# Performance work log

Hardware: AMD Instinct MI355X
Metric: run time of the kernel (lower is better)

Reference implementation:

```python
import jax, jax.numpy as jnp
import numpy as np

D = 1024  # d_model

def setup_inputs() -> dict:
    key = jax.random.key(0)
    ks = jax.random.split(key, 12)
    s = 1.0 / np.sqrt(D)  # torch Linear default init scale
    inp = {
        "q": jax.random.normal(ks[0], (4, 4096, D), dtype=jnp.float32),
        "k": jax.random.normal(ks[1], (4, 4096, D), dtype=jnp.float32),
        "v": jax.random.normal(ks[2], (4, 4096, D), dtype=jnp.float32),
        "Wq": jax.random.uniform(ks[3], (D, D), jnp.float32, -s, s),
        "bq": jax.random.uniform(ks[4], (D,), jnp.float32, -s, s),
        "Wk": jax.random.uniform(ks[5], (D, D), jnp.float32, -s, s),
        "bk": jax.random.uniform(ks[6], (D,), jnp.float32, -s, s),
        "Wv": jax.random.uniform(ks[7], (D, D), jnp.float32, -s, s),
        "bv": jax.random.uniform(ks[8], (D,), jnp.float32, -s, s),
        "Wo": jax.random.uniform(ks[9], (D, D), jnp.float32, -s, s),
        "bo": jax.random.uniform(ks[10], (D,), jnp.float32, -s, s),
    }
    return inp

def reference(q, k, v, Wq, bq, Wk, bk, Wv, bv, Wo, bo):
    # phi feature map: exp(-x^2 / 2)
    phi = lambda x: jnp.exp(-0.5 * x * x)
    Q = phi(q @ Wq.T + bq)            # [B, N, D]
    K = phi(k @ Wk.T + bk)            # [B, N, D]
    V = v @ Wv.T + bv                 # [B, N, D]
    # linear attention: aggregate K^T V once, then contract with Q
    KV = jnp.einsum('bnd,bnl->bdl', K, V)                 # [B, D, D]
    Z = 1.0 / (jnp.einsum('bnd,bd->bn', Q, K.sum(axis=1)) + 1e-6)  # [B, N]
    out = jnp.einsum('bnd,bdl->bnl', Q, KV) * Z[..., None]         # [B, N, D]
    return out @ Wo.T + bo
```

## Files before the change

kernel.cpp:

```cpp
#include <hip/hip_runtime.h>

typedef unsigned short u16;
typedef unsigned int u32;
typedef unsigned long long u64;

typedef __attribute__((ext_vector_type(8))) short short8;
typedef __attribute__((ext_vector_type(4))) float floatx4;

__device__ __forceinline__ float b2f(u16 h) {
  u32 u = ((u32)h) << 16;
  return __builtin_bit_cast(float, u);
}
__device__ __forceinline__ u16 f2b(float f) {
  u32 u = __builtin_bit_cast(u32, f);
  u32 r = 0x7FFFu + ((u >> 16) & 1u);
  return (u16)((u + r) >> 16);
}

__device__ __forceinline__ void gl_lds16(const void* g, void* l) {
  __builtin_amdgcn_global_load_lds(
      (__attribute__((address_space(1))) void*)(u64)g,
      (__attribute__((address_space(3))) void*)(u32)(u64)l, 16, 0, 0);
}

enum { EPI_PHI_BIAS = 0, EPI_BIAS = 1, EPI_NONE = 2,
       EPI_ZBIAS_F32 = 3 };

template<int EPI, bool TRANS_OUT>
__global__ __launch_bounds__(512, 2)
void gemm_bt256(const u16* __restrict__ Ap, const u16* __restrict__ Bp0,
                const float* __restrict__ bias, const float* __restrict__ Zall,
                void* __restrict__ Cp,
                int M, int N, int K, int ldA, int ldB, int ldC,
                long sAb, long sBb, long sCb, long sZb, int abmask, int kshift)
{
  constexpr int TSTRIDE = 65536;
  constexpr int BOFF    = 32768;
  __shared__ char smem[2 * TSTRIDE];

  const int tid  = threadIdx.x;
  const int lane = tid & 63;
  const int wave = tid >> 6;
  const int wm = wave >> 2, wn = wave & 3;
  const int fl = lane & 15;
  const int q  = lane >> 4;
  const int r4 = q * 4;
  const int bm0 = blockIdx.x * 256, bn0 = blockIdx.y * 256;
  const int bz = blockIdx.z;
  const int abz = bz & abmask;
  const int kbase = (bz >> kshift) * K;

  const u16* Ah = Ap  + (size_t)abz * sAb + kbase;
  const u16* Bh = Bp0 + (size_t)abz * sBb + kbase;

  const u16* gA[4]; const u16* gB[4]; int sL[4];
  #pragma unroll
  for (int n = 0; n < 4; ++n) {
    int j = n * 512 + tid;
    int R = j >> 3, c = (j & 7) ^ (R & 7);
    gA[n] = Ah + (size_t)(bm0 + R) * ldA + c * 8;
    gB[n] = Bh + (size_t)(bn0 + R) * ldB + c * 8;
    sL[n] = (n * 512 + wave * 64) * 16;
  }

  int aoff[8], boff[4];
  #pragma unroll
  for (int i = 0; i < 8; ++i) {
    int ra = wm * 128 + i * 16 + fl;
    aoff[i] = ra * 128 + ((q ^ (ra & 7)) * 16);
  }
  #pragma unroll
  for (int i = 0; i < 4; ++i) {
    int rb = wn * 64 + i * 16 + fl;
    boff[i] = rb * 128 + ((q ^ (rb & 7)) * 16);
  }

  floatx4 zero = {0.f, 0.f, 0.f, 0.f};
  floatx4 acc[8][4];
  #pragma unroll
  for (int i = 0; i < 8; ++i)
    #pragma unroll
    for (int j = 0; j < 4; ++j) acc[i][j] = zero;

  auto stage = [&](int t, char* base) {
    int k0 = t * 64;
    #pragma unroll
    for (int n = 0; n < 4; ++n) gl_lds16(gA[n] + k0, base + sL[n]);
    #pragma unroll
    for (int n = 0; n < 4; ++n) gl_lds16(gB[n] + k0, base + BOFF + sL[n]);
  };

  const int NT = K >> 6;
  stage(0, smem);
  asm volatile("s_waitcnt vmcnt(0)\ns_barrier" ::: "memory");
  int cur = 0;
  for (int t = 0; t < NT; ++t) {
    const bool pf = t + 1 < NT;
    const char* bufc = smem + cur;
    char* stb = smem + (cur ^ TSTRIDE);
    const int k1 = (t + 1) * 64;
    short8 aL[8], aH[8], b01[4], b23[4];

    #pragma unroll
    for (int i = 0; i < 4; ++i) {
      aL[2 * i]     = *(const short8*)(bufc + aoff[i]);
      aL[2 * i + 1] = *(const short8*)(bufc + (aoff[i] ^ 64));
    }
    #pragma unroll
    for (int i = 0; i < 2; ++i) {
      b01[2 * i]     = *(const short8*)(bufc + BOFF + boff[i]);
      b01[2 * i + 1] = *(const short8*)(bufc + BOFF + (boff[i] ^ 64));
    }
    if (pf) {
      #pragma unroll
      for (int n = 0; n < 4; ++n) gl_lds16(gA[n] + k1, stb + sL[n]);
    }
    __builtin_amdgcn_s_barrier();
    asm volatile("s_waitcnt lgkmcnt(0)" ::: "memory");
    __builtin_amdgcn_sched_barrier(0);
    __builtin_amdgcn_s_setprio(1);
    #pragma unroll
    for (int kk = 0; kk < 2; ++kk)
      #pragma unroll
      for (int mi = 0; mi < 4; ++mi)
        #pragma unroll
        for (int ni = 0; ni < 2; ++ni)
          acc[mi][ni] = __builtin_amdgcn_mfma_f32_16x16x32_bf16(
              aL[2 * mi + kk], b01[2 * ni + kk], acc[mi][ni], 0, 0, 0);
    __builtin_amdgcn_s_setprio(0);
    __builtin_amdgcn_s_barrier();

    #pragma unroll
    for (int i = 0; i < 2; ++i) {
      b23[2 * i]     = *(const short8*)(bufc + BOFF + boff[i + 2]);
      b23[2 * i + 1] = *(const short8*)(bufc + BOFF + (boff[i + 2] ^ 64));
    }
    if (pf) {
      #pragma unroll
      for (int n = 0; n < 4; ++n) gl_lds16(gB[n] + k1, stb + BOFF + sL[n]);
    }
    __builtin_amdgcn_s_barrier();
    asm volatile("s_waitcnt lgkmcnt(0)" ::: "memory");
    __builtin_amdgcn_sched_barrier(0);
    __builtin_amdgcn_s_setprio(1);
    #pragma unroll
    for (int kk = 0; kk < 2; ++kk)
      #pragma unroll
      for (int mi = 0; mi < 4; ++mi)
        #pragma unroll
        for (int ni = 0; ni < 2; ++ni)
          acc[mi][ni + 2] = __builtin_amdgcn_mfma_f32_16x16x32_bf16(
              aL[2 * mi + kk], b23[2 * ni + kk], acc[mi][ni + 2], 0, 0, 0);
    __builtin_amdgcn_s_setprio(0);
    __builtin_amdgcn_s_barrier();

    #pragma unroll
    for (int i = 0; i < 4; ++i) {
      aH[2 * i]     = *(const short8*)(bufc + aoff[i + 4]);
      aH[2 * i + 1] = *(const short8*)(bufc + (aoff[i + 4] ^ 64));
    }
    __builtin_amdgcn_s_barrier();
    asm volatile("s_waitcnt lgkmcnt(0)" ::: "memory");
    __builtin_amdgcn_sched_barrier(0);
    __builtin_amdgcn_s_setprio(1);
    #pragma unroll
    for (int kk = 0; kk < 2; ++kk)
      #pragma unroll
      for (int mi = 0; mi < 4; ++mi)
        #pragma unroll
        for (int ni = 0; ni < 2; ++ni)
          acc[mi + 4][ni + 2] = __builtin_amdgcn_mfma_f32_16x16x32_bf16(
              aH[2 * mi + kk], b23[2 * ni + kk], acc[mi + 4][ni + 2], 0, 0, 0);
    __builtin_amdgcn_s_setprio(0);
    __builtin_amdgcn_s_barrier();

    __builtin_amdgcn_s_setprio(1);
    #pragma unroll
    for (int kk = 0; kk < 2; ++kk)
      #pragma unroll
      for (int mi = 0; mi < 4; ++mi)
        #pragma unroll
        for (int ni = 0; ni < 2; ++ni)
          acc[mi + 4][ni] = __builtin_amdgcn_mfma_f32_16x16x32_bf16(
              aH[2 * mi + kk], b01[2 * ni + kk], acc[mi + 4][ni], 0, 0, 0);
    __builtin_amdgcn_s_setprio(0);
    if (pf)
      asm volatile("s_waitcnt vmcnt(0) lgkmcnt(0)\ns_barrier" ::: "memory");
    cur ^= TSTRIDE;
  }

  if constexpr (!TRANS_OUT) {
    #pragma unroll
    for (int mi = 0; mi < 8; ++mi) {
      #pragma unroll
      for (int ni = 0; ni < 4; ++ni) {
        int col = bn0 + wn * 64 + ni * 16 + fl;
        #pragma unroll
        for (int r = 0; r < 4; ++r) {
          int row = bm0 + wm * 128 + mi * 16 + r4 + r;
          float vv = acc[mi][ni][r];
          if constexpr (EPI == EPI_PHI_BIAS) {
            vv += bias[col];
            vv = __expf(-0.5f * vv * vv);
          }
          if constexpr (EPI == EPI_ZBIAS_F32)
            vv = vv * Zall[(size_t)abz * sZb + row] + bias[col];
          if constexpr (EPI == EPI_ZBIAS_F32)
            ((float*)Cp)[(size_t)bz * sCb + (size_t)row * ldC + col] = vv;
          else
            ((u16*)Cp)[(size_t)bz * sCb + (size_t)row * ldC + col] = f2b(vv);
        }
      }
    }
  } else {
    u16* sT = (u16*)smem;
    #pragma unroll
    for (int p = 0; p < 2; ++p) {
      __syncthreads();
      if ((wn >> 1) == p) {
        #pragma unroll
        for (int mi = 0; mi < 8; ++mi) {
          #pragma unroll
          for (int ni = 0; ni < 4; ++ni) {
            int colL = wn * 64 + ni * 16 + fl;
            int row0 = wm * 128 + mi * 16 + r4;
            float bcol = bias[bn0 + colL];
            ushort4 h;
            #pragma unroll
            for (int r = 0; r < 4; ++r) {
              float vv = acc[mi][ni][r] + bcol;
              if constexpr (EPI == EPI_PHI_BIAS) vv = __expf(-0.5f * vv * vv);
              ((u16*)&h)[r] = f2b(vv);
            }
            *(ushort4*)(sT + (colL - p * 128) * 264 + row0) = h;
          }
        }
      }
      __syncthreads();
      #pragma unroll
      for (int i = 0; i < 8; ++i) {
        int c = tid + i * 512;
        int dloc = c >> 5, t8 = (c & 31) * 8;
        int4 vv = *(const int4*)(sT + dloc * 264 + t8);
        int gd = bn0 + p * 128 + dloc;
        int gt = bm0 + t8;
        int batch = gt >> 12, tt = gt & 4095;
        *(int4*)((u16*)Cp + ((size_t)batch * N + gd) * 4096 + tt) = vv;
      }
    }
  }
}

__global__ __launch_bounds__(256)
void fcvt(const float* __restrict__ src, u16* __restrict__ dst) {
  size_t i = ((size_t)blockIdx.x * 256 + threadIdx.x) * 8;
  float4 a = *(const float4*)(src + i);
  float4 b = *(const float4*)(src + i + 4);
  union { ushort4 h[2]; int4 v; } o;
  o.h[0].x = f2b(a.x); o.h[0].y = f2b(a.y); o.h[0].z = f2b(a.z); o.h[0].w = f2b(a.w);
  o.h[1].x = f2b(b.x); o.h[1].y = f2b(b.y); o.h[1].z = f2b(b.z); o.h[1].w = f2b(b.w);
  *(int4*)(dst + i) = o.v;
}

__global__ __launch_bounds__(256)
void wconv(const float* __restrict__ w0, const float* __restrict__ w1,
           const float* __restrict__ w2, const float* __restrict__ w3,
           u16* __restrict__ dst) {
  unsigned e = blockIdx.x * 256 + threadIdx.x;
  int mat = e >> 18;
  size_t off = (size_t)(e & 262143) * 4;
  const float* src = mat == 0 ? w0 : mat == 1 ? w1 : mat == 2 ? w2 : w3;
  float4 v = *(const float4*)(src + off);
  ushort4 h;
  h.x = f2b(v.x); h.y = f2b(v.y); h.z = f2b(v.z); h.w = f2b(v.w);
  *(ushort4*)(dst + (size_t)mat * 1048576 + off) = h;
}

__global__ __launch_bounds__(256)
void reduce4(const u16* __restrict__ P, u16* __restrict__ out) {
  size_t i = ((size_t)blockIdx.x * 256 + threadIdx.x) * 8;
  int4 a = *(const int4*)(P + i);
  int4 b = *(const int4*)(P + i + 4194304);
  int4 c = *(const int4*)(P + i + 8388608);
  int4 d = *(const int4*)(P + i + 12582912);
  const u16* ha = (const u16*)&a; const u16* hb = (const u16*)&b;
  const u16* hc = (const u16*)&c; const u16* hd = (const u16*)&d;
  ushort4 o0, o1;
  #pragma unroll
  for (int j = 0; j < 8; ++j) {
    float s = b2f(ha[j]) + b2f(hb[j]) + b2f(hc[j]) + b2f(hd[j]);
    ((u16*)(j < 4 ? &o0 : &o1))[j & 3] = f2b(s);
  }
  *(ushort4*)(out + i) = o0;
  *(ushort4*)(out + i + 4) = o1;
}

__global__ __launch_bounds__(256)
void ksum_rows(const u16* __restrict__ KT, float* __restrict__ Ksum) {
  int lane = threadIdx.x & 63;
  int row = blockIdx.x * 4 + (threadIdx.x >> 6);
  const u16* p = KT + (size_t)row * 4096;
  float s = 0.f;
  #pragma unroll
  for (int i = 0; i < 8; ++i) {
    int4 d = *(const int4*)(p + i * 512 + lane * 8);
    const u16* h = (const u16*)&d;
    #pragma unroll
    for (int j = 0; j < 8; ++j) s += b2f(h[j]);
  }
  #pragma unroll
  for (int off = 32; off; off >>= 1) s += __shfl_xor(s, off, 64);
  if (lane == 0) Ksum[row] = s;
}

__global__ __launch_bounds__(256)
void zden(const u16* __restrict__ Qb, const float* __restrict__ Ksum,
          float* __restrict__ Z) {
  int lane = threadIdx.x & 63;
  int t = blockIdx.x * 4 + (threadIdx.x >> 6);
  const u16* qp = Qb + (size_t)t * 1024;
  const float* ks = Ksum + (size_t)(t >> 12) * 1024;
  float s = 0.f;
  #pragma unroll
  for (int i = 0; i < 2; ++i) {
    int idx = i * 512 + lane * 8;
    int4 d = *(const int4*)(qp + idx);
    const u16* h = (const u16*)&d;
    float4 k0 = *(const float4*)(ks + idx);
    float4 k1 = *(const float4*)(ks + idx + 4);
    s += b2f(h[0]) * k0.x + b2f(h[1]) * k0.y + b2f(h[2]) * k0.z + b2f(h[3]) * k0.w
       + b2f(h[4]) * k1.x + b2f(h[5]) * k1.y + b2f(h[6]) * k1.z + b2f(h[7]) * k1.w;
  }
  #pragma unroll
  for (int off = 32; off; off >>= 1) s += __shfl_xor(s, off, 64);
  if (lane == 0) Z[t] = 1.0f / (s + 1e-6f);
}

extern "C" void kernel_launch(void* const* d_in, const int* in_sizes, int n_in,
                              void* d_out, int out_size, void* d_ws, size_t ws_size,
                              hipStream_t stream) {
  const float* q  = (const float*)d_in[0];
  const float* k  = (const float*)d_in[1];
  const float* v  = (const float*)d_in[2];
  const float* Wq = (const float*)d_in[3];
  const float* bq = (const float*)d_in[4];
  const float* Wk = (const float*)d_in[5];
  const float* bk = (const float*)d_in[6];
  const float* Wv = (const float*)d_in[7];
  const float* bv = (const float*)d_in[8];
  const float* Wo = (const float*)d_in[9];
  const float* bo = (const float*)d_in[10];
  float* out = (float*)d_out;

  u16* Wqb = (u16*)d_ws;
  u16* Wkb = Wqb + 1048576;
  u16* Wvb = Wkb + 1048576;
  u16* Wob = Wvb + 1048576;
  u16* Qb  = Wob + 1048576;
  u16* KT  = Qb  + 16777216;
  u16* VT  = KT  + 16777216;
  u16* KVr = VT  + 16777216;
  float* Ksum = (float*)(KVr + 4194304);
  float* Z    = Ksum + 4096;
  u16* kb16 = Qb;
  u16* vb16 = Qb;
  u16* Pkv  = Qb;
  u16* Pg   = VT;
  u16* Gp   = KT;
  u16* qb16 = VT;

  wconv<<<4096, 256, 0, stream>>>(Wq, Wk, Wv, Wo, Wqb);
  fcvt<<<8192, 256, 0, stream>>>(k, kb16);

  dim3 gp(64, 4, 1);
  gemm_bt256<EPI_PHI_BIAS, true><<<gp, 512, 0, stream>>>(
      kb16, Wkb, bk, nullptr, KT, 16384, 1024, 1024, 1024, 1024, 0,
      0, 0, 0, 0, 0, 2);
  ksum_rows<<<1024, 256, 0, stream>>>(KT, Ksum);

  fcvt<<<8192, 256, 0, stream>>>(v, vb16);
  gemm_bt256<EPI_BIAS, true><<<gp, 512, 0, stream>>>(
      vb16, Wvb, bv, nullptr, VT, 16384, 1024, 1024, 1024, 1024, 0,
      0, 0, 0, 0, 0, 2);

  dim3 g2(4, 4, 16);
  gemm_bt256<EPI_NONE, false><<<g2, 512, 0, stream>>>(
      KT, VT, nullptr, nullptr, Pkv, 1024, 1024, 1024, 4096, 4096, 1024,
      4194304L, 4194304L, 1048576L, 0, 3, 2);
  reduce4<<<2048, 256, 0, stream>>>(Pkv, KVr);

  dim3 gg(4, 4, 16);
  gemm_bt256<EPI_NONE, false><<<gg, 512, 0, stream>>>(
      Wob, KVr, nullptr, nullptr, Pg, 1024, 1024, 256, 1024, 1024, 1024,
      0L, 1048576L, 1048576L, 0, 3, 2);
  reduce4<<<2048, 256, 0, stream>>>(Pg, Gp);

  fcvt<<<8192, 256, 0, stream>>>(q, qb16);
  gemm_bt256<EPI_PHI_BIAS, false><<<gp, 512, 0, stream>>>(
      qb16, Wqb, bq, nullptr, Qb, 16384, 1024, 1024, 1024, 1024, 1024,
      0, 0, 0, 0, 0, 2);
  zden<<<4096, 256, 0, stream>>>(Qb, Ksum, Z);

  dim3 gf(16, 4, 4);
  gemm_bt256<EPI_ZBIAS_F32, false><<<gf, 512, 0, stream>>>(
      Qb, Gp, bo, Z, out, 4096, 1024, 1024, 1024, 1024, 1024,
      4194304L, 1048576L, 4194304L, 4096L, 3, 2);
}
```

Measured before the change: 304.3 us.

## Deepen GEMM prefetch to two tiles ahead with split-phase LDS refills

```diff
diff --git a/kernel.cpp b/kernel.cpp
--- a/kernel.cpp
+++ b/kernel.cpp
@@ -82,23 +82,29 @@
     #pragma unroll
     for (int j = 0; j < 4; ++j) acc[i][j] = zero;
 
-  auto stage = [&](int t, char* base) {
-    int k0 = t * 64;
-    #pragma unroll
-    for (int n = 0; n < 4; ++n) gl_lds16(gA[n] + k0, base + sL[n]);
-    #pragma unroll
-    for (int n = 0; n < 4; ++n) gl_lds16(gB[n] + k0, base + BOFF + sL[n]);
+  auto stA = [&](int t, int n) {
+    gl_lds16(gA[n] + t * 64, smem + (t & 1) * TSTRIDE + sL[n]);
   };
+  auto stB = [&](int t, int n) {
+    gl_lds16(gB[n] + t * 64, smem + (t & 1) * TSTRIDE + BOFF + sL[n]);
+  };
 
   const int NT = K >> 6;
-  stage(0, smem);
-  asm volatile("s_waitcnt vmcnt(0)\ns_barrier" ::: "memory");
-  int cur = 0;
-  for (int t = 0; t < NT; ++t) {
-    const bool pf = t + 1 < NT;
-    const char* bufc = smem + cur;
-    char* stb = smem + (cur ^ TSTRIDE);
-    const int k1 = (t + 1) * 64;
+  #pragma unroll
+  for (int n = 0; n < 4; ++n) stA(0, n);
+  #pragma unroll
+  for (int n = 0; n < 4; ++n) stB(0, n);
+  if (NT > 1) {
+    stA(1, 0); stA(1, 2); stB(1, 0); stB(1, 1); stA(1, 1); stA(1, 3);
+    asm volatile("s_waitcnt vmcnt(6)\ns_barrier" ::: "memory");
+  } else {
+    asm volatile("s_waitcnt vmcnt(0)\ns_barrier" ::: "memory");
+  }
+
+  for (int u = 0; u < NT; ++u) {
+    const bool pf1 = u + 1 < NT;
+    const bool pf2 = u + 2 < NT;
+    const char* bufc = smem + (u & 1) * TSTRIDE;
     short8 aL[8], aH[8], b01[4], b23[4];
 
     #pragma unroll
@@ -111,10 +117,7 @@
       b01[2 * i]     = *(const short8*)(bufc + BOFF + boff[i]);
       b01[2 * i + 1] = *(const short8*)(bufc + BOFF + (boff[i] ^ 64));
     }
-    if (pf) {
-      #pragma unroll
-      for (int n = 0; n < 4; ++n) gl_lds16(gA[n] + k1, stb + sL[n]);
-    }
+    if (pf1) { stB(u + 1, 2); stB(u + 1, 3); }
     __builtin_amdgcn_s_barrier();
     asm volatile("s_waitcnt lgkmcnt(0)" ::: "memory");
     __builtin_amdgcn_sched_barrier(0);
@@ -135,10 +138,7 @@
       b23[2 * i]     = *(const short8*)(bufc + BOFF + boff[i + 2]);
       b23[2 * i + 1] = *(const short8*)(bufc + BOFF + (boff[i + 2] ^ 64));
     }
-    if (pf) {
-      #pragma unroll
-      for (int n = 0; n < 4; ++n) gl_lds16(gB[n] + k1, stb + BOFF + sL[n]);
-    }
+    if (pf2) { stA(u + 2, 0); stA(u + 2, 2); }
     __builtin_amdgcn_s_barrier();
     asm volatile("s_waitcnt lgkmcnt(0)" ::: "memory");
     __builtin_amdgcn_sched_barrier(0);
@@ -159,6 +159,7 @@
       aH[2 * i]     = *(const short8*)(bufc + aoff[i + 4]);
       aH[2 * i + 1] = *(const short8*)(bufc + (aoff[i + 4] ^ 64));
     }
+    if (pf2) { stB(u + 2, 0); stB(u + 2, 1); }
     __builtin_amdgcn_s_barrier();
     asm volatile("s_waitcnt lgkmcnt(0)" ::: "memory");
     __builtin_amdgcn_sched_barrier(0);
@@ -174,6 +175,7 @@
     __builtin_amdgcn_s_setprio(0);
     __builtin_amdgcn_s_barrier();
 
+    if (pf2) { stA(u + 2, 1); stA(u + 2, 3); }
     __builtin_amdgcn_s_setprio(1);
     #pragma unroll
     for (int kk = 0; kk < 2; ++kk)
@@ -184,9 +186,10 @@
           acc[mi + 4][ni] = __builtin_amdgcn_mfma_f32_16x16x32_bf16(
               aH[2 * mi + kk], b01[2 * ni + kk], acc[mi + 4][ni], 0, 0, 0);
     __builtin_amdgcn_s_setprio(0);
-    if (pf)
-      asm volatile("s_waitcnt vmcnt(0) lgkmcnt(0)\ns_barrier" ::: "memory");
-    cur ^= TSTRIDE;
+    if (pf1) {
+      if (pf2) asm volatile("s_waitcnt vmcnt(6) lgkmcnt(0)\ns_barrier" ::: "memory");
+      else     asm volatile("s_waitcnt vmcnt(0) lgkmcnt(0)\ns_barrier" ::: "memory");
+    }
   }
 
   if constexpr (!TRANS_OUT) {
```

After: 302.8 us. Within noise of the previous version (-0.5%).
